# Optimization experiments

Hardware: AMD Instinct MI355X
Metric: run time of the kernel (lower is better)

Reference implementation:

```python
import jax, jax.numpy as jnp
import numpy as np

B, T, C, HS = 1024, 256, 384, 64

def setup_inputs() -> dict:
    key = jax.random.key(0)
    kx, kq, kk, kv = jax.random.split(key, 4)
    x = jax.random.normal(kx, (B, T, C), dtype=jnp.float32)
    # torch Linear(no bias): y = x @ W.T with W [hs, C]; store transposed [C, hs]
    s = 1.0 / np.sqrt(C)
    Wq = jax.random.uniform(kq, (C, HS), jnp.float32, -s, s)
    Wk = jax.random.uniform(kk, (C, HS), jnp.float32, -s, s)
    Wv = jax.random.uniform(kv, (C, HS), jnp.float32, -s, s)
    return {"x": x, "Wq": Wq, "Wk": Wk, "Wv": Wv}

def reference(x, Wq, Wk, Wv):
    Tn = x.shape[1]
    hs = Wq.shape[1]
    q = x @ Wq  # [B,T,hs]
    k = x @ Wk
    v = x @ Wv
    scores = jnp.einsum('bqd,bkd->bqk', q, k) * (hs ** -0.5)  # [B,T,T]
    causal = jnp.tril(jnp.ones((Tn, Tn), dtype=bool))
    scores = jnp.where(causal[None, :, :], scores, -jnp.inf)
    wei = jax.nn.softmax(scores, axis=-1)
    out = jnp.einsum('bqk,bkd->bqd', wei, v)  # [B,T,hs]
    return out
```

## Files before the change

kernel.cpp:

```cpp
#include <hip/hip_runtime.h>
#include <hip/hip_bf16.h>

#define TT 256
#define CC 384
#define HSZ 64

typedef __attribute__((ext_vector_type(8))) short bf16x8;
typedef __attribute__((ext_vector_type(4))) float f32x4;

static __device__ __forceinline__ unsigned short f2bf(float f) {
    union { __hip_bfloat16 h; unsigned short u; } cv;
    cv.h = __float2bfloat16(f);
    return cv.u;
}

static __device__ __forceinline__ bf16x8 cvt8(float4 a, float4 b) {
    bf16x8 r;
    r[0] = (short)f2bf(a.x); r[1] = (short)f2bf(a.y);
    r[2] = (short)f2bf(a.z); r[3] = (short)f2bf(a.w);
    r[4] = (short)f2bf(b.x); r[5] = (short)f2bf(b.y);
    r[6] = (short)f2bf(b.z); r[7] = (short)f2bf(b.w);
    return r;
}

__global__ __launch_bounds__(256) void wtrans_kernel(
        const float* __restrict__ Wq,
        const float* __restrict__ Wk,
        const float* __restrict__ Wv,
        unsigned short* __restrict__ Wt) {
    int idx = blockIdx.x * 256 + threadIdx.x;
    if (idx >= 192 * CC) return;
    int n = idx / CC;
    int ck = idx - n * CC;
    const float* W = (n < 64) ? Wq : ((n < 128) ? Wk : Wv);
    Wt[n * CC + ck] = f2bf(W[ck * HSZ + (n & 63)]);
}

__global__ __launch_bounds__(512, 2) void fused_kernel(
        const float* __restrict__ x,
        const unsigned short* __restrict__ Wt,
        float* __restrict__ outp) {
    __shared__ __align__(16) unsigned short k_lds[TT][72];
    __shared__ __align__(16) unsigned short v_lds[HSZ][264];
    __shared__ __align__(16) unsigned short pbuf[8][16][40];

    const int b    = blockIdx.x;
    const int lane = threadIdx.x & 63;
    const int w    = threadIdx.x >> 6;
    const int c    = lane & 15;
    const int quad = lane >> 4;

    const int Rl0 = 16 * w;
    const int Rl1 = 240 - 16 * w;

    f32x4 acc[2][12];
    #pragma unroll
    for (int t = 0; t < 2; ++t)
        #pragma unroll
        for (int n = 0; n < 12; ++n)
            acc[t][n] = (f32x4){0.f, 0.f, 0.f, 0.f};

    const float* xa0 = x + ((size_t)b * TT + Rl0 + c) * CC + quad * 8;
    const float* xa1 = x + ((size_t)b * TT + Rl1 + c) * CC + quad * 8;
    const unsigned short* wb = Wt + c * CC + quad * 8;

    for (int s = 0; s < 12; ++s) {
        float4 a0lo = *(const float4*)(xa0 + s * 32);
        float4 a0hi = *(const float4*)(xa0 + s * 32 + 4);
        float4 a1lo = *(const float4*)(xa1 + s * 32);
        float4 a1hi = *(const float4*)(xa1 + s * 32 + 4);
        bf16x8 a0 = cvt8(a0lo, a0hi);
        bf16x8 a1 = cvt8(a1lo, a1hi);
        #pragma unroll
        for (int n = 0; n < 12; ++n) {
            bf16x8 bf = *(const bf16x8*)(wb + n * 16 * CC + s * 32);
            acc[0][n] = __builtin_amdgcn_mfma_f32_16x16x32_bf16(a0, bf, acc[0][n], 0, 0, 0);
            acc[1][n] = __builtin_amdgcn_mfma_f32_16x16x32_bf16(a1, bf, acc[1][n], 0, 0, 0);
        }
    }

    bf16x8 qf[2][2];
    #pragma unroll
    for (int t = 0; t < 2; ++t) {
        const int lr = (t == 0 ? Rl0 : Rl1) + quad * 4;
        #pragma unroll
        for (int n = 4; n < 8; ++n) {
            const int cg = (n - 4) * 16 + c;
            #pragma unroll
            for (int r = 0; r < 4; ++r)
                k_lds[lr + r][cg] = f2bf(acc[t][n][r]);
        }
        #pragma unroll
        for (int n = 8; n < 12; ++n) {
            const int hsg = (n - 8) * 16 + c;
            ushort4 pk;
            pk.x = f2bf(acc[t][n][0]);
            pk.y = f2bf(acc[t][n][1]);
            pk.z = f2bf(acc[t][n][2]);
            pk.w = f2bf(acc[t][n][3]);
            *(ushort4*)(&v_lds[hsg][lr]) = pk;
        }
        #pragma unroll
        for (int p = 0; p < 2; ++p) {
            #pragma unroll
            for (int n2 = 0; n2 < 2; ++n2) {
                const int n = 2 * p + n2;
                #pragma unroll
                for (int r = 0; r < 4; ++r)
                    pbuf[w][quad * 4 + r][n2 * 16 + c] = f2bf(acc[t][n][r]);
            }
            qf[t][p] = *(const bf16x8*)(&pbuf[w][c][quad * 8]);
        }
    }

    __syncthreads();

    const int mt0 = w;
    const int mt1 = 15 - w;

    f32x4 of[2][4];
    f32x4 mst[2], lst[2];
    #pragma unroll
    for (int i = 0; i < 2; ++i) {
        mst[i] = (f32x4){-1e30f, -1e30f, -1e30f, -1e30f};
        lst[i] = (f32x4){0.f, 0.f, 0.f, 0.f};
        #pragma unroll
        for (int n = 0; n < 4; ++n)
            of[i][n] = (f32x4){0.f, 0.f, 0.f, 0.f};
    }

    const float qscale = 0.18033688011112042f;

    for (int kt = 0; kt < 8; ++kt) {
        if (mt1 < 2 * kt) break;
        const int k0 = kt * 32;

        bf16x8 kf[2][2], vf[4];
        #pragma unroll
        for (int nt = 0; nt < 2; ++nt)
            #pragma unroll
            for (int ks = 0; ks < 2; ++ks)
                kf[nt][ks] = *(const bf16x8*)(&k_lds[k0 + nt * 16 + c][ks * 32 + quad * 8]);
        #pragma unroll
        for (int n = 0; n < 4; ++n)
            vf[n] = *(const bf16x8*)(&v_lds[n * 16 + c][k0 + quad * 8]);

        #pragma unroll
        for (int ti = 0; ti < 2; ++ti) {
            const int mt = (ti == 0) ? mt0 : mt1;
            if (mt < 2 * kt) continue;
            const int rb = mt * 16;

            f32x4 s0 = {0.f, 0.f, 0.f, 0.f}, s1 = {0.f, 0.f, 0.f, 0.f};
            #pragma unroll
            for (int ks = 0; ks < 2; ++ks) {
                s0 = __builtin_amdgcn_mfma_f32_16x16x32_bf16(qf[ti][ks], kf[0][ks], s0, 0, 0, 0);
                s1 = __builtin_amdgcn_mfma_f32_16x16x32_bf16(qf[ti][ks], kf[1][ks], s1, 0, 0, 0);
            }

            f32x4 t0, t1;
            #pragma unroll
            for (int r = 0; r < 4; ++r) { t0[r] = s0[r] * qscale; t1[r] = s1[r] * qscale; }

            if (mt < 2 * kt + 2) {
                #pragma unroll
                for (int r = 0; r < 4; ++r) {
                    const int row = rb + quad * 4 + r;
                    if (k0 + c > row)      t0[r] = -1e30f;
                    if (k0 + 16 + c > row) t1[r] = -1e30f;
                }
            }

            f32x4 mx;
            #pragma unroll
            for (int r = 0; r < 4; ++r) mx[r] = fmaxf(t0[r], t1[r]);
            #pragma unroll
            for (int off = 1; off < 16; off <<= 1)
                #pragma unroll
                for (int r = 0; r < 4; ++r)
                    mx[r] = fmaxf(mx[r], __shfl_xor(mx[r], off, 64));

            f32x4 mnew, alpha, p0, p1, rs;
            #pragma unroll
            for (int r = 0; r < 4; ++r) {
                mnew[r]  = fmaxf(mst[ti][r], mx[r]);
                alpha[r] = exp2f(mst[ti][r] - mnew[r]);
                p0[r]    = exp2f(t0[r] - mnew[r]);
                p1[r]    = exp2f(t1[r] - mnew[r]);
                rs[r]    = p0[r] + p1[r];
                mst[ti][r] = mnew[r];
            }
            #pragma unroll
            for (int off = 1; off < 16; off <<= 1)
                #pragma unroll
                for (int r = 0; r < 4; ++r)
                    rs[r] += __shfl_xor(rs[r], off, 64);
            #pragma unroll
            for (int r = 0; r < 4; ++r)
                lst[ti][r] = lst[ti][r] * alpha[r] + rs[r];

            #pragma unroll
            for (int n = 0; n < 4; ++n)
                #pragma unroll
                for (int r = 0; r < 4; ++r)
                    of[ti][n][r] *= alpha[r];

            #pragma unroll
            for (int r = 0; r < 4; ++r) {
                pbuf[w][quad * 4 + r][c]      = f2bf(p0[r]);
                pbuf[w][quad * 4 + r][16 + c] = f2bf(p1[r]);
            }
            bf16x8 pf = *(const bf16x8*)(&pbuf[w][c][quad * 8]);
            #pragma unroll
            for (int n = 0; n < 4; ++n)
                of[ti][n] = __builtin_amdgcn_mfma_f32_16x16x32_bf16(pf, vf[n], of[ti][n], 0, 0, 0);
        }
    }

    float* ob = outp + (size_t)b * TT * HSZ;
    #pragma unroll
    for (int ti = 0; ti < 2; ++ti) {
        const int rb = ((ti == 0) ? mt0 : mt1) * 16;
        f32x4 inv;
        #pragma unroll
        for (int r = 0; r < 4; ++r) inv[r] = 1.f / lst[ti][r];
        #pragma unroll
        for (int n = 0; n < 4; ++n)
            #pragma unroll
            for (int r = 0; r < 4; ++r)
                ob[(size_t)(rb + quad * 4 + r) * HSZ + n * 16 + c] = of[ti][n][r] * inv[r];
    }
}

extern "C" void kernel_launch(void* const* d_in, const int* in_sizes, int n_in,
                              void* d_out, int out_size, void* d_ws, size_t ws_size,
                              hipStream_t stream) {
    const float* x  = (const float*)d_in[0];
    const float* Wq = (const float*)d_in[1];
    const float* Wk = (const float*)d_in[2];
    const float* Wv = (const float*)d_in[3];
    float* outp = (float*)d_out;

    const int Bn = in_sizes[0] / (TT * CC);

    unsigned short* Wt = (unsigned short*)d_ws;

    hipLaunchKernelGGL(wtrans_kernel, dim3(288), dim3(256), 0, stream, Wq, Wk, Wv, Wt);
    hipLaunchKernelGGL(fused_kernel, dim3(Bn), dim3(512), 0, stream, x, Wt, outp);
}
```

Measured before the change: 660.9 us.

## Transpose attention MFMAs, serialize projection tiles, and raise occupancy to four blocks

The QKV projection now processes the two row tiles one after another with 12 accumulators instead of 24 live at once. It also prefetches the next x slice while converting the current one. Separately, the score and PV MFMAs swap operand order so each lane holds one query row. This makes the softmax max and sum reductions scalar per lane with two cross-quad shuffles instead of four shuffle rounds on four values, and lets output stores be float4 vectorized. Launch bounds raise the target to 4 blocks per CU, which tightens the register budget and risks spills. LDS use is unchanged and may itself cap residency.

Measured after the change: 789.4 us. 1.19x slower.

```diff
diff --git a/kernel.cpp b/kernel.cpp
--- a/kernel.cpp
+++ b/kernel.cpp
@@ -36,7 +36,7 @@
     Wt[n * CC + ck] = f2bf(W[ck * HSZ + (n & 63)]);
 }
 
-__global__ __launch_bounds__(512, 2) void fused_kernel(
+__global__ __launch_bounds__(512, 4) void fused_kernel(
         const float* __restrict__ x,
         const unsigned short* __restrict__ Wt,
         float* __restrict__ outp) {
@@ -50,54 +50,52 @@
     const int c    = lane & 15;
     const int quad = lane >> 4;
 
-    const int Rl0 = 16 * w;
-    const int Rl1 = 240 - 16 * w;
-
-    f32x4 acc[2][12];
-    #pragma unroll
-    for (int t = 0; t < 2; ++t)
-        #pragma unroll
-        for (int n = 0; n < 12; ++n)
-            acc[t][n] = (f32x4){0.f, 0.f, 0.f, 0.f};
-
-    const float* xa0 = x + ((size_t)b * TT + Rl0 + c) * CC + quad * 8;
-    const float* xa1 = x + ((size_t)b * TT + Rl1 + c) * CC + quad * 8;
     const unsigned short* wb = Wt + c * CC + quad * 8;
 
-    for (int s = 0; s < 12; ++s) {
-        float4 a0lo = *(const float4*)(xa0 + s * 32);
-        float4 a0hi = *(const float4*)(xa0 + s * 32 + 4);
-        float4 a1lo = *(const float4*)(xa1 + s * 32);
-        float4 a1hi = *(const float4*)(xa1 + s * 32 + 4);
-        bf16x8 a0 = cvt8(a0lo, a0hi);
-        bf16x8 a1 = cvt8(a1lo, a1hi);
-        #pragma unroll
-        for (int n = 0; n < 12; ++n) {
-            bf16x8 bf = *(const bf16x8*)(wb + n * 16 * CC + s * 32);
-            acc[0][n] = __builtin_amdgcn_mfma_f32_16x16x32_bf16(a0, bf, acc[0][n], 0, 0, 0);
-            acc[1][n] = __builtin_amdgcn_mfma_f32_16x16x32_bf16(a1, bf, acc[1][n], 0, 0, 0);
-        }
-    }
-
     bf16x8 qf[2][2];
+
     #pragma unroll
     for (int t = 0; t < 2; ++t) {
-        const int lr = (t == 0 ? Rl0 : Rl1) + quad * 4;
+        const int R = (t == 0) ? 16 * w : 240 - 16 * w;
+
+        f32x4 acc[12];
+        #pragma unroll
+        for (int n = 0; n < 12; ++n) acc[n] = (f32x4){0.f, 0.f, 0.f, 0.f};
+
+        const float* xa = x + ((size_t)b * TT + R + c) * CC + quad * 8;
+        float4 alo = *(const float4*)(xa);
+        float4 ahi = *(const float4*)(xa + 4);
+
+        #pragma unroll
+        for (int s = 0; s < 12; ++s) {
+            bf16x8 a = cvt8(alo, ahi);
+            if (s < 11) {
+                alo = *(const float4*)(xa + (s + 1) * 32);
+                ahi = *(const float4*)(xa + (s + 1) * 32 + 4);
+            }
+            #pragma unroll
+            for (int n = 0; n < 12; ++n) {
+                bf16x8 bfv = *(const bf16x8*)(wb + n * 16 * CC + s * 32);
+                acc[n] = __builtin_amdgcn_mfma_f32_16x16x32_bf16(a, bfv, acc[n], 0, 0, 0);
+            }
+        }
+
+        const int lr = R + quad * 4;
         #pragma unroll
         for (int n = 4; n < 8; ++n) {
             const int cg = (n - 4) * 16 + c;
             #pragma unroll
             for (int r = 0; r < 4; ++r)
-                k_lds[lr + r][cg] = f2bf(acc[t][n][r]);
+                k_lds[lr + r][cg] = f2bf(acc[n][r]);
         }
         #pragma unroll
         for (int n = 8; n < 12; ++n) {
             const int hsg = (n - 8) * 16 + c;
             ushort4 pk;
-            pk.x = f2bf(acc[t][n][0]);
-            pk.y = f2bf(acc[t][n][1]);
-            pk.z = f2bf(acc[t][n][2]);
-            pk.w = f2bf(acc[t][n][3]);
+            pk.x = f2bf(acc[n][0]);
+            pk.y = f2bf(acc[n][1]);
+            pk.z = f2bf(acc[n][2]);
+            pk.w = f2bf(acc[n][3]);
             *(ushort4*)(&v_lds[hsg][lr]) = pk;
         }
         #pragma unroll
@@ -107,7 +105,7 @@
                 const int n = 2 * p + n2;
                 #pragma unroll
                 for (int r = 0; r < 4; ++r)
-                    pbuf[w][quad * 4 + r][n2 * 16 + c] = f2bf(acc[t][n][r]);
+                    pbuf[w][quad * 4 + r][n2 * 16 + c] = f2bf(acc[n][r]);
             }
             qf[t][p] = *(const bf16x8*)(&pbuf[w][c][quad * 8]);
         }
@@ -119,15 +117,13 @@
     const int mt1 = 15 - w;
 
     f32x4 of[2][4];
-    f32x4 mst[2], lst[2];
+    float mst[2] = {-1e30f, -1e30f};
+    float lst[2] = {0.f, 0.f};
     #pragma unroll
-    for (int i = 0; i < 2; ++i) {
-        mst[i] = (f32x4){-1e30f, -1e30f, -1e30f, -1e30f};
-        lst[i] = (f32x4){0.f, 0.f, 0.f, 0.f};
+    for (int i = 0; i < 2; ++i)
         #pragma unroll
         for (int n = 0; n < 4; ++n)
             of[i][n] = (f32x4){0.f, 0.f, 0.f, 0.f};
-    }
 
     const float qscale = 0.18033688011112042f;
 
@@ -147,88 +143,84 @@
 
         #pragma unroll
         for (int ti = 0; ti < 2; ++ti) {
-            const int mt = (ti == 0) ? mt0 : mt1;
+            const int mt = ti ? mt1 : mt0;
             if (mt < 2 * kt) continue;
             const int rb = mt * 16;
 
             f32x4 s0 = {0.f, 0.f, 0.f, 0.f}, s1 = {0.f, 0.f, 0.f, 0.f};
             #pragma unroll
             for (int ks = 0; ks < 2; ++ks) {
-                s0 = __builtin_amdgcn_mfma_f32_16x16x32_bf16(qf[ti][ks], kf[0][ks], s0, 0, 0, 0);
-                s1 = __builtin_amdgcn_mfma_f32_16x16x32_bf16(qf[ti][ks], kf[1][ks], s1, 0, 0, 0);
-            }
-
-            f32x4 t0, t1;
+                s0 = __builtin_amdgcn_mfma_f32_16x16x32_bf16(kf[0][ks], qf[ti][ks], s0, 0, 0, 0);
+                s1 = __builtin_amdgcn_mfma_f32_16x16x32_bf16(kf[1][ks], qf[ti][ks], s1, 0, 0, 0);
+            }
+
+            float t0[4], t1[4];
             #pragma unroll
             for (int r = 0; r < 4; ++r) { t0[r] = s0[r] * qscale; t1[r] = s1[r] * qscale; }
 
             if (mt < 2 * kt + 2) {
                 #pragma unroll
                 for (int r = 0; r < 4; ++r) {
-                    const int row = rb + quad * 4 + r;
-                    if (k0 + c > row)      t0[r] = -1e30f;
-                    if (k0 + 16 + c > row) t1[r] = -1e30f;
+                    const int kk = k0 + quad * 4 + r;
+                    if (kk > rb + c)      t0[r] = -1e30f;
+                    if (kk + 16 > rb + c) t1[r] = -1e30f;
                 }
             }
 
-            f32x4 mx;
-            #pragma unroll
-            for (int r = 0; r < 4; ++r) mx[r] = fmaxf(t0[r], t1[r]);
-            #pragma unroll
-            for (int off = 1; off < 16; off <<= 1)
-                #pragma unroll
-                for (int r = 0; r < 4; ++r)
-                    mx[r] = fmaxf(mx[r], __shfl_xor(mx[r], off, 64));
-
-            f32x4 mnew, alpha, p0, p1, rs;
+            float mx = fmaxf(fmaxf(fmaxf(t0[0], t0[1]), fmaxf(t0[2], t0[3])),
+                             fmaxf(fmaxf(t1[0], t1[1]), fmaxf(t1[2], t1[3])));
+            mx = fmaxf(mx, __shfl_xor(mx, 16, 64));
+            mx = fmaxf(mx, __shfl_xor(mx, 32, 64));
+
+            const float mnew  = fmaxf(mst[ti], mx);
+            const float alpha = exp2f(mst[ti] - mnew);
+            mst[ti] = mnew;
+
+            float p0[4], p1[4];
+            float rs = 0.f;
             #pragma unroll
             for (int r = 0; r < 4; ++r) {
-                mnew[r]  = fmaxf(mst[ti][r], mx[r]);
-                alpha[r] = exp2f(mst[ti][r] - mnew[r]);
-                p0[r]    = exp2f(t0[r] - mnew[r]);
-                p1[r]    = exp2f(t1[r] - mnew[r]);
-                rs[r]    = p0[r] + p1[r];
-                mst[ti][r] = mnew[r];
-            }
-            #pragma unroll
-            for (int off = 1; off < 16; off <<= 1)
-                #pragma unroll
-                for (int r = 0; r < 4; ++r)
-                    rs[r] += __shfl_xor(rs[r], off, 64);
-            #pragma unroll
-            for (int r = 0; r < 4; ++r)
-                lst[ti][r] = lst[ti][r] * alpha[r] + rs[r];
+                p0[r] = exp2f(t0[r] - mnew);
+                p1[r] = exp2f(t1[r] - mnew);
+                rs += p0[r] + p1[r];
+            }
+            rs += __shfl_xor(rs, 16, 64);
+            rs += __shfl_xor(rs, 32, 64);
+            lst[ti] = lst[ti] * alpha + rs;
 
             #pragma unroll
             for (int n = 0; n < 4; ++n)
                 #pragma unroll
                 for (int r = 0; r < 4; ++r)
-                    of[ti][n][r] *= alpha[r];
-
-            #pragma unroll
-            for (int r = 0; r < 4; ++r) {
-                pbuf[w][quad * 4 + r][c]      = f2bf(p0[r]);
-                pbuf[w][quad * 4 + r][16 + c] = f2bf(p1[r]);
-            }
+                    of[ti][n][r] *= alpha;
+
+            ushort4 pk0, pk1;
+            pk0.x = f2bf(p0[0]); pk0.y = f2bf(p0[1]); pk0.z = f2bf(p0[2]); pk0.w = f2bf(p0[3]);
+            pk1.x = f2bf(p1[0]); pk1.y = f2bf(p1[1]); pk1.z = f2bf(p1[2]); pk1.w = f2bf(p1[3]);
+            *(ushort4*)(&pbuf[w][c][quad * 4])      = pk0;
+            *(ushort4*)(&pbuf[w][c][16 + quad * 4]) = pk1;
             bf16x8 pf = *(const bf16x8*)(&pbuf[w][c][quad * 8]);
+
             #pragma unroll
             for (int n = 0; n < 4; ++n)
-                of[ti][n] = __builtin_amdgcn_mfma_f32_16x16x32_bf16(pf, vf[n], of[ti][n], 0, 0, 0);
+                of[ti][n] = __builtin_amdgcn_mfma_f32_16x16x32_bf16(vf[n], pf, of[ti][n], 0, 0, 0);
         }
     }
 
     float* ob = outp + (size_t)b * TT * HSZ;
     #pragma unroll
     for (int ti = 0; ti < 2; ++ti) {
-        const int rb = ((ti == 0) ? mt0 : mt1) * 16;
-        f32x4 inv;
-        #pragma unroll
-        for (int r = 0; r < 4; ++r) inv[r] = 1.f / lst[ti][r];
-        #pragma unroll
-        for (int n = 0; n < 4; ++n)
-            #pragma unroll
-            for (int r = 0; r < 4; ++r)
-                ob[(size_t)(rb + quad * 4 + r) * HSZ + n * 16 + c] = of[ti][n][r] * inv[r];
+        const int rb = (ti ? mt1 : mt0) * 16;
+        const float inv = 1.f / lst[ti];
+        #pragma unroll
+        for (int n = 0; n < 4; ++n) {
+            float4 st;
+            st.x = of[ti][n][0] * inv;
+            st.y = of[ti][n][1] * inv;
+            st.z = of[ti][n][2] * inv;
+            st.w = of[ti][n][3] * inv;
+            *(float4*)(ob + (size_t)(rb + c) * HSZ + n * 16 + quad * 4) = st;
+        }
     }
 }
 
```
